# Optimization experiments

Measured on AMD Instinct MI355X. Metric: run time of the kernel, lower is better.

The kernel has to match this reference:

```python
import jax, jax.numpy as jnp
import numpy as np

# ---- static anchor construction (mirrors build_anchors + valid_index in __init__) ----
F_W, F_H, F_S = 50, 37, 16
SCALES = (8.0, 16.0, 24.0)
RATIOS = (0.5, 1.0, 2.0)
K1 = 400            # rp() top-k proposals fed to NMS
NMS_THRESH = 0.6
BN_EPS = 1e-5

def _build_anchors():
    anchors = []
    for y in range(F_H):
        for x in range(F_W):
            cx = x * F_S + F_S / 2.0
            cy = y * F_S + F_S / 2.0
            for r in RATIOS:           # 3 ratios x 3 scales = 9 anchors/cell (18 = 9*2 cls ch)
                for s in SCALES:
                    h = F_S * s * np.sqrt(r)
                    w = F_S * s / np.sqrt(r)
                    anchors.append([cx - w / 2, cy - h / 2, cx + w / 2, cy + h / 2])
    return np.asarray(anchors, dtype=np.float32)

_ANCH = _build_anchors()
_VALID = np.where((_ANCH[:, 0] >= 0) & (_ANCH[:, 1] >= 0) &
                  (_ANCH[:, 2] < F_W * F_S) & (_ANCH[:, 3] < F_H * F_S))[0]
VALID_ANCHOR = jnp.asarray(_ANCH[_VALID])   # [V, 4]
VALID_INDEX = jnp.asarray(_VALID)            # [V]


def _conv(x, w, b, pad):
    y = jax.lax.conv_general_dilated(x, w, (1, 1), [(pad, pad), (pad, pad)],
                                     dimension_numbers=('NCHW', 'OIHW', 'NCHW'))
    return y + b[None, :, None, None]


def _nms_keep(boxes, scores, thresh):
    """Greedy NMS over K1 boxes; returns bool keep mask aligned to input order."""
    n = boxes.shape[0]
    order = jnp.argsort(-scores)
    b = boxes[order]
    x1, y1, x2, y2 = b[:, 0], b[:, 1], b[:, 2], b[:, 3]
    area = (x2 - x1 + 1.0) * (y2 - y1 + 1.0)
    iw = jnp.clip(jnp.minimum(x2[:, None], x2[None, :]) - jnp.maximum(x1[:, None], x1[None, :]) + 1.0, 0.0)
    ih = jnp.clip(jnp.minimum(y2[:, None], y2[None, :]) - jnp.maximum(y1[:, None], y1[None, :]) + 1.0, 0.0)
    inter = iw * ih
    iou = inter / (area[:, None] + area[None, :] - inter)
    idx = jnp.arange(n)

    def body(i, supp):
        alive = ~supp[i]
        new = alive & (iou[i] > thresh) & (idx > i)
        return supp | new

    supp = jax.lax.fori_loop(0, n, body, jnp.zeros(n, dtype=bool))
    return jnp.zeros(n, dtype=bool).at[order].set(~supp)


def _rp_single(off_i, cls_i):
    """rp(): softmax fg score -> top-k1 -> box decode -> NMS keep mask."""
    off_v = off_i[VALID_INDEX]                       # [V, 4]
    cls_v = cls_i[VALID_INDEX]                       # [V, 2]
    score = jax.nn.softmax(cls_v, axis=1)[:, 1]
    top_s, top_idx = jax.lax.top_k(score, K1)
    a = VALID_ANCHOR[top_idx]
    t = off_v[top_idx]
    xa = (a[:, 0] + a[:, 2]) / 2
    ya = (a[:, 1] + a[:, 3]) / 2
    wa = a[:, 2] - a[:, 0] + 1.0
    ha = a[:, 3] - a[:, 1] + 1.0
    x = t[:, 0] * wa + xa
    y = t[:, 1] * ha + ya
    w = wa * jnp.exp(t[:, 2])
    h = ha * jnp.exp(t[:, 3])
    boxes = jnp.stack([x - w / 2, y - h / 2, x + w / 2, y + h / 2], axis=1)  # [K1, 4]
    keep = _nms_keep(jnp.trunc(boxes), top_s, NMS_THRESH)  # original casts to int before NMS
    return boxes, keep


def setup_inputs() -> dict:
    key = jax.random.key(0)
    ks = jax.random.split(key, 8)
    B = 8
    return {
        'feature': jax.random.normal(ks[0], (B, 512, F_H, F_W), jnp.float32),
        'md_w': jax.random.normal(ks[1], (512, 512, 3, 3), jnp.float32) * 0.02,
        'md_b': jax.random.normal(ks[2], (512,), jnp.float32) * 0.01,
        'bn_gamma': jnp.ones((512,), jnp.float32),
        'bn_beta': jnp.zeros((512,), jnp.float32),
        'cls_w': jax.random.normal(ks[3], (18, 512, 1, 1), jnp.float32) * 0.02,
        'cls_b': jax.random.normal(ks[4], (18,), jnp.float32) * 0.01,
        'off_w': jax.random.normal(ks[5], (36, 512, 1, 1), jnp.float32) * 0.02,
        'off_b': jax.random.normal(ks[6], (36,), jnp.float32) * 0.01,
    }


def reference(feature, md_w, md_b, bn_gamma, bn_beta, cls_w, cls_b, off_w, off_b):
    B = feature.shape[0]
    # more_deep: Conv3x3 -> BatchNorm (training-mode batch stats) -> ReLU
    out = _conv(feature, md_w, md_b, pad=1)
    mean = out.mean(axis=(0, 2, 3), keepdims=True)
    var = out.var(axis=(0, 2, 3), keepdims=True)
    out = bn_gamma[None, :, None, None] * (out - mean) * jax.lax.rsqrt(var + BN_EPS) + bn_beta[None, :, None, None]
    out = jax.nn.relu(out)
    # 1x1 heads, then permute(0,2,3,1).reshape as in predict()
    cls = _conv(out, cls_w, cls_b, pad=0)   # [B,18,H,W]
    off = _conv(out, off_w, off_b, pad=0)   # [B,36,H,W]
    cls_pred = cls.transpose(0, 2, 3, 1).reshape(B, -1, 2)   # [B, H*W*9, 2]
    offset_pred = off.transpose(0, 2, 3, 1).reshape(B, -1, 4)  # [B, H*W*9, 4]
    boxes, keep = jax.vmap(_rp_single)(offset_pred, cls_pred)  # [B,K1,4], [B,K1] bool
    return offset_pred, cls_pred, boxes, keep
```

## Files before the change

kernel.cpp:

```cpp
#include <hip/hip_runtime.h>
#include <cstdint>

#define BHW_ 14800
#define CHW_ 947200
#define A_   16650
#define OCLS 532800
#define OBOX 799200
#define OKEEP 812000
#define NSTEP 144

typedef unsigned int u32;
typedef unsigned long long u64;
typedef _Float16 f16x8 __attribute__((ext_vector_type(8)));
typedef float f32x4 __attribute__((ext_vector_type(4)));

union U8 { f16x8 v; u32 u[4]; };
union H2U { _Float16 f; unsigned short u; };

__device__ __forceinline__ unsigned int fkey(float f){
  unsigned int u = __float_as_uint(f);
  return (u & 0x80000000u) ? ~u : (u | 0x80000000u);
}

__device__ __forceinline__ void anchor_corners(int x, int y, int kk,
                                               float& ax1, float& ay1, float& ax2, float& ay2){
  int si = kk % 3, ri = kk / 3;
  double rv = (ri==0) ? 0.5 : ((ri==1) ? 1.0 : 2.0);
  double sr = sqrt(rv);
  double fs = 128.0 * (double)(si+1);
  double h = fs * sr, w = fs / sr;
  double cx = (double)(x*16 + 8), cy = (double)(y*16 + 8);
  ax1 = (float)(cx - w*0.5); ay1 = (float)(cy - h*0.5);
  ax2 = (float)(cx + w*0.5); ay2 = (float)(cy + h*0.5);
}

__global__ __launch_bounds__(256) void k_prep(const float* __restrict__ feat, const float* __restrict__ mdw,
                                              const float* __restrict__ cw, const float* __restrict__ cb,
                                              const float* __restrict__ ow, const float* __restrict__ ob,
                                              u32* __restrict__ Fp, _Float16* __restrict__ WfA,
                                              float* __restrict__ hwp, float* __restrict__ hb,
                                              u64* __restrict__ Sg){
  int bid = blockIdx.x;
  if (bid < 8112){
    int q = bid*256 + threadIdx.x;
    int p4 = (q % 507)*4;
    int bc = q / 507;
    u32 outw[4];
    #pragma unroll
    for (int e = 0; e < 4; ++e){
      int padpos = p4 + e;
      int yp = padpos/52, xp = padpos - yp*52;
      float v = 0.f;
      int y = yp - 1, x = xp - 1;
      if ((unsigned)y < 37u && (unsigned)x < 50u) v = feat[(size_t)bc*1850 + y*50 + x];
      _Float16 h = (_Float16)v;
      _Float16 l = (_Float16)(v - (float)h);
      H2U hu, lu; hu.f = h; lu.f = l;
      outw[e] = ((u32)lu.u << 16) | (u32)hu.u;
    }
    *(uint4*)&Fp[(size_t)bc*2028 + p4] = *(uint4*)outw;
  } else if (bid < 9264){
    int u = (bid - 8112)*256 + threadIdx.x;
    int khw = u % 9;
    int v = u / 9;
    int o7  = v & 127;
    int l4g = (v >> 7) & 3;
    int ot  = (v >> 9) & 3;
    int cc  = v >> 11;
    int o = ot*128 + o7;
    int s = cc*9 + khw;
    f16x8 hi, lo;
    #pragma unroll
    for (int j = 0; j < 8; ++j){
      float val = mdw[(size_t)(o*512 + cc*32 + l4g*8 + j)*9 + khw];
      _Float16 h = (_Float16)val;
      hi[j] = h; lo[j] = (_Float16)(val - (float)h);
    }
    size_t base = ((size_t)(s*4 + ot)*1024 + (size_t)(l4g*2)*128 + o7)*8;
    *(f16x8*)&WfA[base] = hi;
    *(f16x8*)&WfA[base + 1024] = lo;
  } else {
    int t = (bid - 9264)*256 + threadIdx.x;
    if (t < 64) hb[t] = (t < 18) ? cb[t] : (t < 54 ? ob[t-18] : 0.f);
    if (t < 1024) Sg[t] = 0ull;
    int r = t & 63, ci = t >> 6;
    hwp[t] = (r < 18) ? cw[r*512 + ci] : (r < 54 ? ow[(r-18)*512 + ci] : 0.f);
  }
}

__global__ __launch_bounds__(512, 2) void k_conv3_mfma(const u32* __restrict__ Fp,
                                                       const _Float16* __restrict__ WfA,
                                                       const float* __restrict__ mdb,
                                                       float* __restrict__ out0,
                                                       u64* __restrict__ Sg){
  __shared__ _Float16 Abuf[2][8192];
  __shared__ _Float16 Bbuf[2][8192];
  __shared__ u64 Sred[256];
  const int tid = threadIdx.x;
  if (tid < 256) Sred[tid] = 0ull;
  int flat = blockIdx.x;
  int xcd = flat & 7, sub = flat >> 3;
  int swz = xcd * 58 + sub;
  int otile = swz / 116;
  int ntile = swz - otile*116;

  const int bpos = tid & 127, kg8 = tid >> 7;
  int n = ntile*128 + bpos; if (n >= BHW_) n = BHW_ - 1;
  int nb = n/1850; int rem = n - nb*1850; int ny = rem/50; int nx = rem - ny*50;
  const u32* bbase = Fp + (size_t)(nb*512 + kg8*8)*2028 + (ny+1)*52 + (nx+1);

  u32 R[8];
  auto loadB = [&](int s){
    int cc = s/9, khw = s - cc*9;
    int dy = khw/3 - 1, dx = khw - (khw/3)*3 - 1;
    const u32* src = bbase + (size_t)cc*32*2028 + dy*52 + dx;
    #pragma unroll
    for (int i = 0; i < 8; ++i) R[i] = src[(size_t)i*2028];
  };
  auto writeB = [&](int cur){
    U8 hi, lo;
    #pragma unroll
    for (int p = 0; p < 4; ++p){
      u32 P0 = R[2*p], P1 = R[2*p+1];
      hi.u[p] = (P1 << 16) | (P0 & 0xFFFFu);
      lo.u[p] = (P0 >> 16) | (P1 & 0xFFFF0000u);
    }
    *(f16x8*)&Bbuf[cur][(size_t)((kg8*2 + 0)*128 + bpos)*8] = hi.v;
    *(f16x8*)&Bbuf[cur][(size_t)((kg8*2 + 1)*128 + bpos)*8] = lo.v;
  };
  auto stageA = [&](int s, int cur){
    const _Float16* g = WfA + ((size_t)(s*4 + otile)*1024 + tid)*8;
    _Float16* l = &Abuf[cur][(size_t)tid*8];
    __builtin_amdgcn_global_load_lds((const __attribute__((address_space(1))) void*)g,
                                     (__attribute__((address_space(3))) void*)l, 16, 0, 0);
    __builtin_amdgcn_global_load_lds((const __attribute__((address_space(1))) void*)(g + 4096),
                                     (__attribute__((address_space(3))) void*)(l + 4096), 16, 0, 0);
  };

  const int w = tid >> 6, lane = tid & 63;
  const int wm = w >> 2, wn = w & 3;
  const int l15 = lane & 15, l4 = lane >> 4;

  f32x4 acc[4][2] = {};

  auto compute = [&](int cur){
    f16x8 ah[4], al[4], bh[2], bl[2];
    #pragma unroll
    for (int mf = 0; mf < 4; ++mf){
      int m = wm*64 + mf*16 + l15;
      ah[mf] = *(const f16x8*)&Abuf[cur][(size_t)((l4*2 + 0)*128 + m)*8];
      al[mf] = *(const f16x8*)&Abuf[cur][(size_t)((l4*2 + 1)*128 + m)*8];
    }
    #pragma unroll
    for (int nf = 0; nf < 2; ++nf){
      int nn = wn*32 + nf*16 + l15;
      bh[nf] = *(const f16x8*)&Bbuf[cur][(size_t)((l4*2 + 0)*128 + nn)*8];
      bl[nf] = *(const f16x8*)&Bbuf[cur][(size_t)((l4*2 + 1)*128 + nn)*8];
    }
    #pragma unroll
    for (int mf = 0; mf < 4; ++mf)
      #pragma unroll
      for (int nf = 0; nf < 2; ++nf){
        acc[mf][nf] = __builtin_amdgcn_mfma_f32_16x16x32_f16(ah[mf], bh[nf], acc[mf][nf], 0,0,0);
        acc[mf][nf] = __builtin_amdgcn_mfma_f32_16x16x32_f16(ah[mf], bl[nf], acc[mf][nf], 0,0,0);
        acc[mf][nf] = __builtin_amdgcn_mfma_f32_16x16x32_f16(al[mf], bh[nf], acc[mf][nf], 0,0,0);
      }
  };

  loadB(0);
  stageA(0, 0);
  writeB(0);
  __syncthreads();

  int cur = 0;
  for (int s = 0; s < NSTEP; ++s){
    if (s + 1 < NSTEP){
      loadB(s+1);
      stageA(s+1, cur^1);
      __builtin_amdgcn_sched_barrier(0);
    }
    compute(cur);
    if (s + 1 < NSTEP) writeB(cur^1);
    __syncthreads();
    cur ^= 1;
  }

  #pragma unroll
  for (int nf = 0; nf < 2; ++nf){
    int ng = ntile*128 + wn*32 + nf*16 + l15;
    if (ng >= BHW_) continue;
    int b2 = ng/1850; int rem2 = ng - b2*1850;
    #pragma unroll
    for (int mf = 0; mf < 4; ++mf){
      int o0 = otile*128 + wm*64 + mf*16 + l4*4;
      #pragma unroll
      for (int r = 0; r < 4; ++r){
        out0[(size_t)b2*CHW_ + (size_t)(o0 + r)*1850 + rem2] = acc[mf][nf][r] + mdb[o0 + r];
      }
    }
  }
  #pragma unroll
  for (int mf = 0; mf < 4; ++mf){
    int o0 = otile*128 + wm*64 + mf*16 + l4*4;
    #pragma unroll
    for (int r = 0; r < 4; ++r){
      float bias = mdb[o0 + r];
      long long s = 0, s2 = 0;
      #pragma unroll
      for (int nf = 0; nf < 2; ++nf){
        int ng = ntile*128 + wn*32 + nf*16 + l15;
        if (ng < BHW_){
          float v = acc[mf][nf][r] + bias;
          s  += llrintf(v * 16777216.0f);
          s2 += llrintf((v * v) * 1073741824.0f);
        }
      }
      #pragma unroll
      for (int m2 = 1; m2 < 16; m2 <<= 1){
        s  += __shfl_xor(s,  m2, 64);
        s2 += __shfl_xor(s2, m2, 64);
      }
      if (l15 == 0){
        int cloc = wm*64 + mf*16 + l4*4 + r;
        atomicAdd(&Sred[cloc*2],   (u64)s);
        atomicAdd(&Sred[cloc*2+1], (u64)s2);
      }
    }
  }
  __syncthreads();
  if (tid < 256) atomicAdd(&Sg[otile*256 + tid], Sred[tid]);
}

__global__ __launch_bounds__(256) void k_heads(const float* __restrict__ out0, const float* __restrict__ hwp,
                                               const float* __restrict__ hb, const u64* __restrict__ Sg,
                                               const float* __restrict__ gamma,
                                               const float* __restrict__ beta, float* __restrict__ dout,
                                               u64* __restrict__ keys){
#pragma clang fp contract(off)
  __shared__ float As[16][64];
  __shared__ float Bs[16][32];
  __shared__ float bnmL[512], bnrL[512];
  __shared__ int sb[32], sy[32], sx[32];
  int tid = threadIdx.x; int ntile = blockIdx.x;
  for (int c = tid; c < 512; c += 256){
    double s  = (double)(long long)Sg[c*2]   / 16777216.0;
    double s2 = (double)(long long)Sg[c*2+1] / 1073741824.0;
    double m = s / 14800.0;
    double var = s2 / 14800.0 - m*m;
    bnmL[c] = (float)m;
    bnrL[c] = 1.0f / sqrtf((float)var + 1e-5f);
  }
  if (tid < 32){
    int n = ntile*32 + tid;
    if (n < BHW_){ int b = n/1850; int r = n - b*1850; int y = r/50; sb[tid]=b; sy[tid]=y; sx[tid]=r - y*50; }
    else { sb[tid] = -1; sy[tid] = 0; sx[tid] = 0; }
  }
  __syncthreads();
  float acc[4][2] = {};
  const int tx = tid & 15, ty = tid >> 4;
  const int lci = tid >> 4, lo4 = (tid & 15) * 4, lo2 = (tid & 15) * 2;
  for (int ct = 0; ct < 32; ++ct){
    int cib = ct*16;
    float4 av = *(const float4*)(hwp + (cib + lci)*64 + lo4);
    float2 bv; float* bp = (float*)&bv;
    int cig = cib + lci;
    float gm = gamma[cig], mm = bnmL[cig], rr = bnrL[cig], bt = beta[cig];
    #pragma unroll
    for (int j = 0; j < 2; ++j){
      int nn = lo2 + j; int b = sb[nn];
      float v = 0.f;
      if (b >= 0){
        float x = out0[(size_t)b*CHW_ + (size_t)cig*1850 + sy[nn]*50 + sx[nn]];
        float y = gm * (x - mm);
        y = y * rr;
        y = y + bt;
        v = fmaxf(y, 0.f);
      }
      bp[j] = v;
    }
    __syncthreads();
    *(float4*)&As[lci][lo4] = av;
    *(float2*)&Bs[lci][lo2] = bv;
    __syncthreads();
    #pragma unroll
    for (int k = 0; k < 16; ++k){
      float4 a4 = *(const float4*)&As[k][ty*4];
      float2 b2 = *(const float2*)&Bs[k][tx*2];
      const float* ap = (const float*)&a4; const float* bq = (const float*)&b2;
      #pragma unroll
      for (int i = 0; i < 4; ++i)
        #pragma unroll
        for (int j = 0; j < 2; ++j)
          acc[i][j] = fmaf(ap[i], bq[j], acc[i][j]);
    }
  }
  #pragma unroll
  for (int i = 0; i < 4; ++i){
    int r = ty*4 + i;
    if (r >= 54) continue;
    float bias = hb[r];
    #pragma unroll
    for (int j = 0; j < 2; ++j){
      int nl = tx*2 + j;
      int b = sb[nl];
      if (b < 0) continue;
      int pos = sy[nl]*50 + sx[nl];
      float v = acc[i][j] + bias;
      if (r < 18){
        int kk = r >> 1, cc = r & 1;
        dout[OCLS + ((size_t)b*A_ + pos*9 + kk)*2 + cc] = v;
      } else {
        int r2 = r - 18, kk = r2 >> 2, cc = r2 & 3;
        dout[((size_t)b*A_ + pos*9 + kk)*4 + cc] = v;
      }
    }
  }
  if (ty < 5){
    #pragma unroll
    for (int i = 0; i < 4; i += 2){
      int r = ty*4 + i;
      if (r >= 18) continue;
      int kk = r >> 1;
      float b0 = hb[r], b1 = hb[r+1];
      #pragma unroll
      for (int j = 0; j < 2; ++j){
        int nl = tx*2 + j;
        int b = sb[nl];
        if (b < 0) continue;
        float c0 = acc[i][j] + b0;
        float c1 = acc[i+1][j] + b1;
        float d = c1 - c0;
        float ax1, ay1, ax2, ay2;
        anchor_corners(sx[nl], sy[nl], kk, ax1, ay1, ax2, ay2);
        bool valid = (ax1 >= 0.f) && (ay1 >= 0.f) && (ax2 < 800.f) && (ay2 < 592.f);
        unsigned a = (unsigned)(sy[nl]*50 + sx[nl])*9u + (unsigned)kk;
        u64 key = valid ? (((u64)fkey(d) << 32) | (u64)(~a)) : 0ull;
        keys[(size_t)b*A_ + a] = key;
      }
    }
  }
}

__global__ __launch_bounds__(1024) void k_post(const u64* __restrict__ keys,
                                               float* __restrict__ dout){
#pragma clang fp contract(off)
  __shared__ u32 hist[4096];
  __shared__ u32 sp[1024];
  __shared__ u64 selbuf[4096];
  __shared__ u64 stopk[400];
  __shared__ u32 adj32[6400];
  __shared__ float X1[400], Y1[400], X2[400], Y2[400], AR[400];
  __shared__ u32 ssup[13];
  __shared__ u32 s_t1, s_base1, s_t2, scnt;
  int b = blockIdx.x, tid = threadIdx.x;
  const u64* kb = keys + (size_t)b*A_;

  for (int i = tid; i < 4096; i += 1024) hist[i] = 0u;
  if (tid == 0) scnt = 0u;
  __syncthreads();
  for (int i = tid; i < A_; i += 1024){
    u64 k = kb[i];
    if (k) atomicAdd(&hist[(u32)(k >> 52)], 1u);
  }
  __syncthreads();
  {
    u32 p = hist[tid*4] + hist[tid*4+1] + hist[tid*4+2] + hist[tid*4+3];
    sp[tid] = p; __syncthreads();
    for (int off = 1; off < 1024; off <<= 1){
      u32 v = sp[tid] + ((tid + off < 1024) ? sp[tid + off] : 0u);
      __syncthreads(); sp[tid] = v; __syncthreads();
    }
    if (sp[tid] >= 400u && (tid == 1023 || sp[tid+1] < 400u)){
      u32 cum = (tid == 1023) ? 0u : sp[tid+1];
      for (int bb = tid*4 + 3; bb >= tid*4; --bb){
        cum += hist[bb];
        if (cum >= 400u){ s_t1 = (u32)bb; s_base1 = cum - hist[bb]; break; }
      }
    }
  }
  __syncthreads();
  const u32 t1 = s_t1;
  const u32 need2 = 400u - s_base1;

  __syncthreads();
  for (int i = tid; i < 4096; i += 1024) hist[i] = 0u;
  __syncthreads();
  for (int i = tid; i < A_; i += 1024){
    u64 k = kb[i];
    if (k && (u32)(k >> 52) == t1) atomicAdd(&hist[(u32)(k >> 40) & 0xFFFu], 1u);
  }
  __syncthreads();
  {
    u32 p = hist[tid*4] + hist[tid*4+1] + hist[tid*4+2] + hist[tid*4+3];
    sp[tid] = p; __syncthreads();
    for (int off = 1; off < 1024; off <<= 1){
      u32 v = sp[tid] + ((tid + off < 1024) ? sp[tid + off] : 0u);
      __syncthreads(); sp[tid] = v; __syncthreads();
    }
    if (sp[tid] >= need2 && (tid == 1023 || sp[tid+1] < need2)){
      u32 cum = (tid == 1023) ? 0u : sp[tid+1];
      for (int bb = tid*4 + 3; bb >= tid*4; --bb){
        cum += hist[bb];
        if (cum >= need2){ s_t2 = (u32)bb; break; }
      }
    }
  }
  __syncthreads();
  const u32 t2 = s_t2;

  for (int i = tid; i < A_; i += 1024){
    u64 k = kb[i];
    if (!k) continue;
    u32 top = (u32)(k >> 52);
    bool sel = (top > t1) || (top == t1 && ((u32)(k >> 40) & 0xFFFu) >= t2);
    if (sel){
      u32 pidx = atomicAdd(&scnt, 1u);
      if (pidx < 4096u) selbuf[pidx] = k;
    }
  }
  __syncthreads();
  int C = min((int)scnt, 4096);

  for (int i = tid; i < C; i += 1024){
    u64 my = selbuf[i];
    int c = 0;
    for (int j = 0; j < C; ++j) c += (selbuf[j] > my) ? 1 : 0;
    if (c < 400) stopk[c] = my;
  }
  __syncthreads();

  for (int i = tid; i < 6400; i += 1024) adj32[i] = 0u;
  if (tid < 400){
    u64 key = stopk[tid];
    unsigned a = ~(unsigned)(key & 0xFFFFFFFFull);
    int pos = a/9; int kk = a - pos*9;
    int y = pos/50; int x = pos - y*50;
    float ax1, ay1, ax2, ay2;
    anchor_corners(x, y, kk, ax1, ay1, ax2, ay2);
    float xa = (ax1 + ax2) * 0.5f;
    float ya = (ay1 + ay2) * 0.5f;
    float wa = ax2 - ax1 + 1.0f;
    float ha = ay2 - ay1 + 1.0f;
    const float* t = dout + ((size_t)b*A_ + a)*4;
    float t0 = t[0], t1f = t[1], t2f = t[2], t3 = t[3];
    float xc = t0 * wa + xa;
    float yc = t1f * ha + ya;
    float bw = wa * expf(t2f);
    float bh = ha * expf(t3);
    float bx1 = xc - bw*0.5f, by1 = yc - bh*0.5f;
    float bx2 = xc + bw*0.5f, by2 = yc + bh*0.5f;
    float* bo = dout + OBOX + ((size_t)b*400 + tid)*4;
    bo[0] = bx1; bo[1] = by1; bo[2] = bx2; bo[3] = by2;
    float tx1 = truncf(bx1), ty1 = truncf(by1), tx2 = truncf(bx2), ty2 = truncf(by2);
    X1[tid] = tx1; Y1[tid] = ty1; X2[tid] = tx2; Y2[tid] = ty2;
    AR[tid] = (tx2 - tx1 + 1.0f) * (ty2 - ty1 + 1.0f);
  }
  __syncthreads();
  for (int q = tid; q < 160000; q += 1024){
    int i = q / 400, j = q - i*400;
    if (j > i){
      float iw = fminf(X2[i], X2[j]) - fmaxf(X1[i], X1[j]) + 1.0f; iw = fmaxf(iw, 0.f);
      float ih = fminf(Y2[i], Y2[j]) - fmaxf(Y1[i], Y1[j]) + 1.0f; ih = fmaxf(ih, 0.f);
      float inter = iw * ih;
      float iou = inter / ((AR[i] + AR[j]) - inter);
      if (iou > 0.6f) atomicOr(&adj32[i*16 + (j >> 5)], 1u << (j & 31));
    }
  }
  __syncthreads();
  if (tid < 64){
    u32 sup = 0;
    for (int i = 0; i < 399; ++i){
      u32 a = (tid < 13) ? adj32[i*16 + tid] : 0u;
      u32 so = __shfl(sup, i >> 5);
      if (!((so >> (i & 31)) & 1u)) sup |= a;
    }
    if (tid < 13) ssup[tid] = sup;
  }
  __syncthreads();
  if (tid < 400)
    dout[OKEEP + (size_t)b*400 + tid] = ((ssup[tid >> 5] >> (tid & 31)) & 1u) ? 0.f : 1.f;
}

extern "C" void kernel_launch(void* const* d_in, const int* in_sizes, int n_in,
                              void* d_out, int out_size, void* d_ws, size_t ws_size,
                              hipStream_t stream){
  const float* feat  = (const float*)d_in[0];
  const float* mdw   = (const float*)d_in[1];
  const float* mdb   = (const float*)d_in[2];
  const float* gamma = (const float*)d_in[3];
  const float* beta  = (const float*)d_in[4];
  const float* clsw  = (const float*)d_in[5];
  const float* clsb  = (const float*)d_in[6];
  const float* offw  = (const float*)d_in[7];
  const float* offb  = (const float*)d_in[8];
  float* dout = (float*)d_out;
  float* ws = (float*)d_ws;

  float* out0 = ws;
  _Float16* WfA = (_Float16*)(out0 + 7577600);
  u32* Fp = (u32*)(out0 + 7577600 + 2359296);
  float* hwp = (float*)(Fp + 8306688);
  float* hb  = hwp + 32768;
  u64* Sg = (u64*)(hb + 64);
  u64* keys = Sg + 1024;

  k_prep<<<dim3(9392), 256, 0, stream>>>(feat, mdw, clsw, clsb, offw, offb, Fp, WfA, hwp, hb, Sg);
  k_conv3_mfma<<<dim3(464), 512, 0, stream>>>(Fp, WfA, mdb, out0, Sg);
  k_heads<<<dim3(463), 256, 0, stream>>>(out0, hwp, hb, Sg, gamma, beta, dout, keys);
  k_post<<<dim3(8), 1024, 0, stream>>>(keys, dout);
}
```

Baseline: 364.1 us.

## Load conv weight fragments directly into registers instead of staging through LDS

The A (weight) operand of the 3x3 conv MFMA loop is no longer staged into shared memory with global_load_lds. Each wave now loads its fragments straight from global memory into registers, double-buffered across even and odd steps with a 2x unrolled loop. This halves LDS use per block and raises the launch-bounds occupancy hint from 2 to 4 blocks per CU. The cost is more VGPR pressure and redundant global/L2 reads of weights across waves sharing the same rows, and the higher occupancy target may force register spills.

After: 711.2 us. +95.3%, slower.

```diff
diff --git a/kernel.cpp b/kernel.cpp
--- a/kernel.cpp
+++ b/kernel.cpp
@@ -88,12 +88,11 @@
   }
 }
 
-__global__ __launch_bounds__(512, 2) void k_conv3_mfma(const u32* __restrict__ Fp,
+__global__ __launch_bounds__(512, 4) void k_conv3_mfma(const u32* __restrict__ Fp,
                                                        const _Float16* __restrict__ WfA,
                                                        const float* __restrict__ mdb,
                                                        float* __restrict__ out0,
                                                        u64* __restrict__ Sg){
-  __shared__ _Float16 Abuf[2][8192];
   __shared__ _Float16 Bbuf[2][8192];
   __shared__ u64 Sred[256];
   const int tid = threadIdx.x;
@@ -128,29 +127,27 @@
     *(f16x8*)&Bbuf[cur][(size_t)((kg8*2 + 0)*128 + bpos)*8] = hi.v;
     *(f16x8*)&Bbuf[cur][(size_t)((kg8*2 + 1)*128 + bpos)*8] = lo.v;
   };
-  auto stageA = [&](int s, int cur){
-    const _Float16* g = WfA + ((size_t)(s*4 + otile)*1024 + tid)*8;
-    _Float16* l = &Abuf[cur][(size_t)tid*8];
-    __builtin_amdgcn_global_load_lds((const __attribute__((address_space(1))) void*)g,
-                                     (__attribute__((address_space(3))) void*)l, 16, 0, 0);
-    __builtin_amdgcn_global_load_lds((const __attribute__((address_space(1))) void*)(g + 4096),
-                                     (__attribute__((address_space(3))) void*)(l + 4096), 16, 0, 0);
-  };
 
   const int w = tid >> 6, lane = tid & 63;
   const int wm = w >> 2, wn = w & 3;
   const int l15 = lane & 15, l4 = lane >> 4;
 
+  const f16x8* Af = (const f16x8*)WfA;
+  const size_t abase = (size_t)otile*1024 + (size_t)(l4*2)*128 + wm*64 + l15;
+
+  auto loadA = [&](int s, f16x8* ah, f16x8* al){
+    const f16x8* p = Af + abase + (size_t)s*4096;
+    #pragma unroll
+    for (int mf = 0; mf < 4; ++mf){
+      ah[mf] = p[mf*16];
+      al[mf] = p[mf*16 + 128];
+    }
+  };
+
   f32x4 acc[4][2] = {};
 
-  auto compute = [&](int cur){
-    f16x8 ah[4], al[4], bh[2], bl[2];
-    #pragma unroll
-    for (int mf = 0; mf < 4; ++mf){
-      int m = wm*64 + mf*16 + l15;
-      ah[mf] = *(const f16x8*)&Abuf[cur][(size_t)((l4*2 + 0)*128 + m)*8];
-      al[mf] = *(const f16x8*)&Abuf[cur][(size_t)((l4*2 + 1)*128 + m)*8];
-    }
+  auto compute = [&](const f16x8* ah, const f16x8* al, int cur){
+    f16x8 bh[2], bl[2];
     #pragma unroll
     for (int nf = 0; nf < 2; ++nf){
       int nn = wn*32 + nf*16 + l15;
@@ -167,20 +164,31 @@
       }
   };
 
+  f16x8 ahE[4], alE[4], ahO[4], alO[4];
+
   loadB(0);
-  stageA(0, 0);
+  loadA(0, ahE, alE);
   writeB(0);
   __syncthreads();
 
   int cur = 0;
-  for (int s = 0; s < NSTEP; ++s){
+  for (int s = 0; s < NSTEP; s += 2){
     if (s + 1 < NSTEP){
       loadB(s+1);
-      stageA(s+1, cur^1);
+      loadA(s+1, ahO, alO);
       __builtin_amdgcn_sched_barrier(0);
     }
-    compute(cur);
+    compute(ahE, alE, cur);
     if (s + 1 < NSTEP) writeB(cur^1);
+    __syncthreads();
+    cur ^= 1;
+    if (s + 2 < NSTEP){
+      loadB(s+2);
+      loadA(s+2, ahE, alE);
+      __builtin_amdgcn_sched_barrier(0);
+    }
+    compute(ahO, alO, cur);
+    if (s + 2 < NSTEP) writeB(cur^1);
     __syncthreads();
     cur ^= 1;
   }
```
